# Kernel tuning notes

Hardware: AMD Instinct MI355X
Metric: run time of the kernel (lower is better)

## Reference

```python
import jax, jax.numpy as jnp
import numpy as np

N_EMBED = 1024
E_DIM = 256
BETA = 0.25


def setup_inputs() -> dict:
    key = jax.random.key(0)
    k1, k2 = jax.random.split(key)
    z = jax.random.normal(k1, (32, 16, 16, 16, E_DIM), dtype=jnp.float32)
    emb = jax.random.normal(k2, (N_EMBED, E_DIM), dtype=jnp.float32)
    return {"z": z, "emb": emb}


def reference(z, emb):
    sg = jax.lax.stop_gradient
    z_flat = z.reshape(-1, E_DIM)                      # [N, e_dim]
    similarity = z_flat @ emb.T                        # [N, n_embed]
    codebook_idxs = jnp.argmax(similarity, axis=-1)    # [N]
    z_q = emb[codebook_idxs].reshape(z.shape)          # gather nearest code
    vq_loss = jnp.mean((z_q - sg(z)) ** 2)
    commitment_loss = BETA * jnp.mean((sg(z_q) - z) ** 2)
    z_q = z + sg(z_q - z)                              # straight-through
    return (z_q, vq_loss, commitment_loss, codebook_idxs)
```

## Files before the change

### kernel.cpp

```cpp
#include <hip/hip_runtime.h>

#define E_DIM  256
#define NC     1024
#define BM     128
#define BN     128
#define NT     512
#define LDBS   72
#define MARGIN 0.02f

typedef short  bf16x4 __attribute__((ext_vector_type(4)));
typedef short  bf16x8 __attribute__((ext_vector_type(8)));
typedef float  f32x4  __attribute__((ext_vector_type(4)));

static __device__ __forceinline__ void split2(float x, short& hi, short& lo) {
    const unsigned u  = __float_as_uint(x);
    const unsigned hb = (u + 0x7FFFu + ((u >> 16) & 1u)) >> 16;
    hi = (short)hb;
    const float l = x - __uint_as_float(hb << 16);
    const unsigned u2 = __float_as_uint(l);
    lo = (short)((u2 + 0x7FFFu + ((u2 >> 16) & 1u)) >> 16);
}

static __device__ __forceinline__ float mkey(float v, unsigned il) {
    return __uint_as_float((__float_as_uint(v) & 0xFFFFFC00u) | il);
}

__global__ __launch_bounds__(NT, 2) void vq_kernel(
    const float* __restrict__ z, const float* __restrict__ emb,
    float* __restrict__ zq, float* __restrict__ loss,
    float* __restrict__ idxf, float invN)
{
    __shared__ short Bs_hi[BN * LDBS];
    __shared__ short Bs_lo[BN * LDBS];
    __shared__ float topk[2][BM][2];
    __shared__ int   rowIdx[BM];
    __shared__ int   ambList[BM];
    __shared__ int   ambCnt;
    __shared__ float zs[E_DIM];
    __shared__ float redV[8];
    __shared__ int   redI[8];

    const int tid  = threadIdx.x;
    const int lane = tid & 63;
    const int w    = tid >> 6;
    const int wm   = w >> 1;
    const int wn   = w & 1;
    const int l15  = lane & 15;
    const int l4   = lane >> 4;
    const int rb   = blockIdx.x * BM;

    bf16x8 a_hi[2][8], a_lo[2][8];
#pragma unroll
    for (int m = 0; m < 2; ++m) {
        const float* zp = &z[(size_t)(rb + wm * 32 + m * 16 + l15) * E_DIM + l4 * 8];
#pragma unroll
        for (int s = 0; s < 8; ++s) {
            const f32x4 x0 = *reinterpret_cast<const f32x4*>(&zp[s * 32]);
            const f32x4 x1 = *reinterpret_cast<const f32x4*>(&zp[s * 32 + 4]);
            bf16x8 h, l; short hh, ll;
#pragma unroll
            for (int j = 0; j < 4; ++j) { split2(x0[j], hh, ll); h[j]   = hh; l[j]   = ll; }
#pragma unroll
            for (int j = 0; j < 4; ++j) { split2(x1[j], hh, ll); h[4+j] = hh; l[4+j] = ll; }
            a_hi[m][s] = h; a_lo[m][s] = l;
        }
    }

    float k1[2][4], k2[2][4];
#pragma unroll
    for (int m = 0; m < 2; ++m)
#pragma unroll
        for (int j = 0; j < 4; ++j) { k1[m][j] = -3.0e38f; k2[m][j] = -3.0e38f; }

    for (int cn = 0; cn < NC; cn += BN) {
        f32x4 acc[2][4];
        const f32x4 zz = {0.f, 0.f, 0.f, 0.f};
#pragma unroll
        for (int m = 0; m < 2; ++m)
#pragma unroll
            for (int n = 0; n < 4; ++n) acc[m][n] = zz;

#pragma unroll
        for (int kk = 0; kk < 4; ++kk) {
            __syncthreads();
#pragma unroll
            for (int i = 0; i < 4; ++i) {
                const int q   = i * NT + tid;
                const int row = q >> 4;
                const int c   = q & 15;
                const f32x4 b4 = *reinterpret_cast<const f32x4*>(
                    &emb[(size_t)(cn + row) * E_DIM + kk * 64 + c * 4]);
                bf16x4 hv, lv; short hh, ll;
#pragma unroll
                for (int j = 0; j < 4; ++j) { split2(b4[j], hh, ll); hv[j] = hh; lv[j] = ll; }
                *reinterpret_cast<bf16x4*>(&Bs_hi[row * LDBS + c * 4]) = hv;
                *reinterpret_cast<bf16x4*>(&Bs_lo[row * LDBS + c * 4]) = lv;
            }
            __syncthreads();
#pragma unroll
            for (int h = 0; h < 2; ++h) {
                bf16x8 bh[4], bl[4];
#pragma unroll
                for (int n = 0; n < 4; ++n) {
                    const int off = (wn * 64 + n * 16 + l15) * LDBS + (h * 4 + l4) * 8;
                    bh[n] = *reinterpret_cast<const bf16x8*>(&Bs_hi[off]);
                    bl[n] = *reinterpret_cast<const bf16x8*>(&Bs_lo[off]);
                }
#pragma unroll
                for (int m = 0; m < 2; ++m) {
                    const bf16x8 ah = a_hi[m][kk * 2 + h];
                    const bf16x8 al = a_lo[m][kk * 2 + h];
#pragma unroll
                    for (int n = 0; n < 4; ++n) {
                        acc[m][n] = __builtin_amdgcn_mfma_f32_16x16x32_bf16(ah, bh[n], acc[m][n], 0, 0, 0);
                        acc[m][n] = __builtin_amdgcn_mfma_f32_16x16x32_bf16(ah, bl[n], acc[m][n], 0, 0, 0);
                        acc[m][n] = __builtin_amdgcn_mfma_f32_16x16x32_bf16(al, bh[n], acc[m][n], 0, 0, 0);
                    }
                }
            }
        }

        const int colbase = cn + wn * 64 + l15;
        unsigned il[4];
#pragma unroll
        for (int n = 0; n < 4; ++n) il[n] = (unsigned)(1023 - (colbase + n * 16));
#pragma unroll
        for (int m = 0; m < 2; ++m)
#pragma unroll
            for (int j = 0; j < 4; ++j) {
                const float a0 = acc[m][0][j], a1 = acc[m][1][j];
                const float a2 = acc[m][2][j], a3 = acc[m][3][j];
                const float q = fmaxf(fmaxf(a0, a1), fmaxf(a2, a3));
                if (q > k2[m][j]) {
                    float x, t;
                    x = mkey(a0, il[0]); t = fminf(k1[m][j], x);
                    k1[m][j] = fmaxf(k1[m][j], x); k2[m][j] = fmaxf(k2[m][j], t);
                    x = mkey(a1, il[1]); t = fminf(k1[m][j], x);
                    k1[m][j] = fmaxf(k1[m][j], x); k2[m][j] = fmaxf(k2[m][j], t);
                    x = mkey(a2, il[2]); t = fminf(k1[m][j], x);
                    k1[m][j] = fmaxf(k1[m][j], x); k2[m][j] = fmaxf(k2[m][j], t);
                    x = mkey(a3, il[3]); t = fminf(k1[m][j], x);
                    k1[m][j] = fmaxf(k1[m][j], x); k2[m][j] = fmaxf(k2[m][j], t);
                }
            }
    }

#pragma unroll
    for (int m = 0; m < 2; ++m)
#pragma unroll
        for (int j = 0; j < 4; ++j) {
            float a = k1[m][j], b = k2[m][j];
#pragma unroll
            for (int s = 1; s < 16; s <<= 1) {
                const float oa = __shfl_xor(a, s, 64);
                const float ob = __shfl_xor(b, s, 64);
                const float t  = fminf(a, oa);
                a = fmaxf(a, oa);
                b = fmaxf(fmaxf(b, ob), t);
            }
            if (l15 == 0) {
                const int row = wm * 32 + m * 16 + l4 * 4 + j;
                topk[wn][row][0] = a;
                topk[wn][row][1] = b;
            }
        }
    if (tid == 0) ambCnt = 0;
    __syncthreads();

    if (tid < BM) {
        float a = topk[0][tid][0], b = topk[0][tid][1];
        const float oa = topk[1][tid][0], ob = topk[1][tid][1];
        const float t  = fminf(a, oa);
        a = fmaxf(a, oa);
        b = fmaxf(fmaxf(b, ob), t);
        const unsigned ub = __float_as_uint(a);
        rowIdx[tid] = 1023 - (int)(ub & 1023u);
        const float v1 = __uint_as_float(ub & 0xFFFFFC00u);
        const float v2 = __uint_as_float(__float_as_uint(b) & 0xFFFFFC00u);
        if (v1 - v2 <= MARGIN) {
            const int p = atomicAdd(&ambCnt, 1);
            ambList[p] = tid;
        }
    }
    __syncthreads();

    const int nAmb = ambCnt;
    for (int ai = 0; ai < nAmb; ++ai) {
        const int row = ambList[ai];
        if (tid < 64)
            *reinterpret_cast<f32x4*>(&zs[tid * 4]) =
                *reinterpret_cast<const f32x4*>(&z[(size_t)(rb + row) * E_DIM + tid * 4]);
        __syncthreads();
        float best = -3.0e38f; int bidx = 0;
#pragma unroll
        for (int cc = 0; cc < 2; ++cc) {
            const int c = tid * 2 + cc;
            const float* ep = &emb[(size_t)c * E_DIM];
            float p = 0.f;
#pragma unroll 8
            for (int qd = 0; qd < 64; ++qd) {
                const f32x4 e4 = *reinterpret_cast<const f32x4*>(&ep[qd * 4]);
                const f32x4 z4 = *reinterpret_cast<const f32x4*>(&zs[qd * 4]);
                p = fmaf(z4[0], e4[0], p); p = fmaf(z4[1], e4[1], p);
                p = fmaf(z4[2], e4[2], p); p = fmaf(z4[3], e4[3], p);
            }
            if (p > best) { best = p; bidx = c; }
        }
#pragma unroll
        for (int s = 1; s < 64; s <<= 1) {
            const float ov = __shfl_xor(best, s, 64);
            const int   oi = __shfl_xor(bidx, s, 64);
            if (ov > best || (ov == best && oi < bidx)) { best = ov; bidx = oi; }
        }
        if (lane == 0) { redV[w] = best; redI[w] = bidx; }
        __syncthreads();
        if (tid == 0) {
            float bb = redV[0]; int bi = redI[0];
#pragma unroll
            for (int ww = 1; ww < 8; ++ww)
                if (redV[ww] > bb) { bb = redV[ww]; bi = redI[ww]; }
            rowIdx[row] = bi;
        }
        __syncthreads();
    }

    float sse = 0.f;
#pragma unroll
    for (int i = 0; i < 16; ++i) {
        const int f   = i * NT + tid;
        const int row = f >> 6;
        const int kq  = f & 63;
        const int idx = rowIdx[row];
        const f32x4 e4 = *reinterpret_cast<const f32x4*>(&emb[(size_t)idx * E_DIM + kq * 4]);
        const f32x4 z4 = *reinterpret_cast<const f32x4*>(&z[(size_t)(rb + row) * E_DIM + kq * 4]);
        const float d0 = e4[0] - z4[0], d1 = e4[1] - z4[1];
        const float d2 = e4[2] - z4[2], d3 = e4[3] - z4[3];
        sse += d0 * d0 + d1 * d1 + d2 * d2 + d3 * d3;
        *reinterpret_cast<f32x4*>(&zq[(size_t)(rb + row) * E_DIM + kq * 4]) = e4;
    }
    if (tid < BM) idxf[rb + tid] = (float)rowIdx[tid];
#pragma unroll
    for (int s = 1; s < 64; s <<= 1) sse += __shfl_xor(sse, s, 64);
    if (lane == 0) redV[w] = sse;
    __syncthreads();
    if (tid == 0) {
        float t = 0.f;
#pragma unroll
        for (int ww = 0; ww < 8; ++ww) t += redV[ww];
        atomicAdd(&loss[0], t * invN);
        atomicAdd(&loss[1], 0.25f * t * invN);
    }
}

extern "C" void kernel_launch(void* const* d_in, const int* in_sizes, int n_in,
                              void* d_out, int out_size, void* d_ws, size_t ws_size,
                              hipStream_t stream) {
    const float* z   = (const float*)d_in[0];
    const float* emb = (const float*)d_in[1];
    const int zsz    = in_sizes[0];
    const int nrows  = zsz / E_DIM;

    float* out  = (float*)d_out;
    float* zq   = out;
    float* loss = out + zsz;
    float* idxf = out + zsz + 2;

    hipMemsetAsync(loss, 0, 2 * sizeof(float), stream);

    vq_kernel<<<dim3(nrows / BM), NT, 0, stream>>>(
        z, emb, zq, loss, idxf, 1.0f / ((float)nrows * (float)E_DIM));
}
```

Baseline: 752.7 us.

## Precompute split-bf16 codebook image and stream it into LDS with double-buffered direct loads

A small prep kernel converts the fp32 codebook once per call into hi/lo bf16 tiles with an XOR-swizzled layout and writes them to workspace. Before this, every block re-read the fp32 codebook and re-ran the split for each tile. The main kernel now copies those pre-laid-out tiles with global_load_lds into a double-buffered 64KB shared array, prefetching the next chunk while computing the current one, and keeps one barrier per chunk instead of two. In exchange it adds an extra launch, relies on the workspace, and raises LDS use, which may limit the occupancy of two blocks per CU.

```diff
diff --git a/kernel.cpp b/kernel.cpp
--- a/kernel.cpp
+++ b/kernel.cpp
@@ -3,9 +3,7 @@
 #define E_DIM  256
 #define NC     1024
 #define BM     128
-#define BN     128
 #define NT     512
-#define LDBS   72
 #define MARGIN 0.02f
 
 typedef short  bf16x4 __attribute__((ext_vector_type(4)));
@@ -25,13 +23,41 @@
     return __uint_as_float((__float_as_uint(v) & 0xFFFFFC00u) | il);
 }
 
+static __device__ __forceinline__ void gload16(const void* g, void* l) {
+    __builtin_amdgcn_global_load_lds(
+        (const __attribute__((address_space(1))) unsigned int*)g,
+        (__attribute__((address_space(3))) unsigned int*)l, 16, 0, 0);
+}
+
+__global__ __launch_bounds__(256) void vq_prep(
+    const float* __restrict__ emb, short* __restrict__ img)
+{
+    const int t     = blockIdx.x * 256 + threadIdx.x;
+    const int b     = t & 7;
+    const int row   = (t >> 3) & 127;
+    const int chunk = (t >> 10) & 3;
+    const int tile  = t >> 12;
+    const int cb    = (b << 4) ^ ((row & 7) << 4);
+    const int s0    = cb >> 1;
+    const float* src = &emb[(size_t)(tile * 128 + row) * E_DIM + chunk * 64 + s0];
+    const f32x4 x0 = *reinterpret_cast<const f32x4*>(&src[0]);
+    const f32x4 x1 = *reinterpret_cast<const f32x4*>(&src[4]);
+    bf16x8 h, l; short hh, ll;
+#pragma unroll
+    for (int j = 0; j < 4; ++j) { split2(x0[j], hh, ll); h[j]     = hh; l[j]     = ll; }
+#pragma unroll
+    for (int j = 0; j < 4; ++j) { split2(x1[j], hh, ll); h[4 + j] = hh; l[4 + j] = ll; }
+    const size_t base = (size_t)(tile * 4 + chunk) * 16384;
+    *reinterpret_cast<bf16x8*>(&img[base + row * 64 + b * 8])        = h;
+    *reinterpret_cast<bf16x8*>(&img[base + 8192 + row * 64 + b * 8]) = l;
+}
+
 __global__ __launch_bounds__(NT, 2) void vq_kernel(
     const float* __restrict__ z, const float* __restrict__ emb,
-    float* __restrict__ zq, float* __restrict__ loss,
-    float* __restrict__ idxf, float invN)
+    const short* __restrict__ img, float* __restrict__ zq,
+    float* __restrict__ loss, float* __restrict__ idxf, float invN)
 {
-    __shared__ short Bs_hi[BN * LDBS];
-    __shared__ short Bs_lo[BN * LDBS];
+    __shared__ char  Bs[2][32768];
     __shared__ float topk[2][BM][2];
     __shared__ int   rowIdx[BM];
     __shared__ int   ambList[BM];
@@ -49,6 +75,15 @@
     const int l4   = lane >> 4;
     const int rb   = blockIdx.x * BM;
 
+    {
+        const char* g = (const char*)img;
+#pragma unroll
+        for (int q = 0; q < 4; ++q) {
+            const int off = (q * 8 + w) * 1024;
+            gload16(g + off + (lane << 4), &Bs[0][off]);
+        }
+    }
+
     bf16x8 a_hi[2][8], a_lo[2][8];
 #pragma unroll
     for (int m = 0; m < 2; ++m) {
@@ -72,7 +107,9 @@
 #pragma unroll
         for (int j = 0; j < 4; ++j) { k1[m][j] = -3.0e38f; k2[m][j] = -3.0e38f; }
 
-    for (int cn = 0; cn < NC; cn += BN) {
+    __syncthreads();
+
+    for (int tile = 0; tile < 8; ++tile) {
         f32x4 acc[2][4];
         const f32x4 zz = {0.f, 0.f, 0.f, 0.f};
 #pragma unroll
@@ -82,29 +119,27 @@
 
 #pragma unroll
         for (int kk = 0; kk < 4; ++kk) {
-            __syncthreads();
-#pragma unroll
-            for (int i = 0; i < 4; ++i) {
-                const int q   = i * NT + tid;
-                const int row = q >> 4;
-                const int c   = q & 15;
-                const f32x4 b4 = *reinterpret_cast<const f32x4*>(
-                    &emb[(size_t)(cn + row) * E_DIM + kk * 64 + c * 4]);
-                bf16x4 hv, lv; short hh, ll;
-#pragma unroll
-                for (int j = 0; j < 4; ++j) { split2(b4[j], hh, ll); hv[j] = hh; lv[j] = ll; }
-                *reinterpret_cast<bf16x4*>(&Bs_hi[row * LDBS + c * 4]) = hv;
-                *reinterpret_cast<bf16x4*>(&Bs_lo[row * LDBS + c * 4]) = lv;
-            }
-            __syncthreads();
+            const int gc  = tile * 4 + kk;
+            const int sgc = (gc < 31) ? gc + 1 : 31;
+            {
+                const char* g = (const char*)img + (size_t)sgc * 32768;
+                char* const db = Bs[(kk + 1) & 1];
+#pragma unroll
+                for (int q = 0; q < 4; ++q) {
+                    const int off = (q * 8 + w) * 1024;
+                    gload16(g + off + (lane << 4), &db[off]);
+                }
+            }
+            const char* bc = Bs[kk & 1];
 #pragma unroll
             for (int h = 0; h < 2; ++h) {
                 bf16x8 bh[4], bl[4];
 #pragma unroll
                 for (int n = 0; n < 4; ++n) {
-                    const int off = (wn * 64 + n * 16 + l15) * LDBS + (h * 4 + l4) * 8;
-                    bh[n] = *reinterpret_cast<const bf16x8*>(&Bs_hi[off]);
-                    bl[n] = *reinterpret_cast<const bf16x8*>(&Bs_lo[off]);
+                    const int row = wn * 64 + n * 16 + l15;
+                    const int off = row * 128 + (((h * 4 + l4) << 4) ^ ((row & 7) << 4));
+                    bh[n] = *reinterpret_cast<const bf16x8*>(&bc[off]);
+                    bl[n] = *reinterpret_cast<const bf16x8*>(&bc[16384 + off]);
                 }
 #pragma unroll
                 for (int m = 0; m < 2; ++m) {
@@ -118,9 +153,10 @@
                     }
                 }
             }
-        }
-
-        const int colbase = cn + wn * 64 + l15;
+            __syncthreads();
+        }
+
+        const int colbase = tile * 128 + wn * 64 + l15;
         unsigned il[4];
 #pragma unroll
         for (int n = 0; n < 4; ++n) il[n] = (unsigned)(1023 - (colbase + n * 16));
@@ -265,8 +301,11 @@
     float* loss = out + zsz;
     float* idxf = out + zsz + 2;
 
+    short* img = (short*)d_ws;
+
     hipMemsetAsync(loss, 0, 2 * sizeof(float), stream);
 
+    vq_prep<<<dim3(128), 256, 0, stream>>>(emb, img);
     vq_kernel<<<dim3(nrows / BM), NT, 0, stream>>>(
-        z, emb, zq, loss, idxf, 1.0f / ((float)nrows * (float)E_DIM));
-}
+        z, emb, img, zq, loss, idxf, 1.0f / ((float)nrows * (float)E_DIM));
+}
```

Result: faster. 632.0 us (-16.0%).
